# Kernel optimization log

Measured on AMD Instinct MI355X. Metric: run time of the kernel, lower is better.

The kernel has to match this reference:

```python
import jax, jax.numpy as jnp
import numpy as np

OS_FACTOR = 2.0  # init kwarg; k = 1/os_factor Euler step size
B, T, IN, H = 32, 4096, 1, 512


def setup_inputs() -> dict:
    key = jax.random.key(0)
    k0, k1, k2, k3, k4 = jax.random.split(key, 5)
    scale = 1.0 / np.sqrt(H).astype(np.float32)
    return {
        "x": jax.random.normal(k0, (B, T, IN), jnp.float32),
        "W_ih": jax.random.uniform(k1, (4 * H, IN), jnp.float32, -scale, scale),
        "W_hh": jax.random.uniform(k2, (4 * H, H), jnp.float32, -scale, scale),
        "b_ih": jax.random.uniform(k3, (4 * H,), jnp.float32, -scale, scale),
        "b_hh": jax.random.uniform(k4, (4 * H,), jnp.float32, -scale, scale),
    }


def reference(x, W_ih, W_hh, b_ih, b_hh):
    """STN_RNN forward with an LSTMCell: h_state <- h_state + k*(cell(x,h_state) - h_state).
    State vector is [h, c] concatenated (state_size = 2H). Returns (states_h, final_state)."""
    k = 1.0 / OS_FACTOR
    h = W_hh.shape[1]
    h0 = jnp.zeros((x.shape[0], 2 * h), x.dtype)

    def step(state, x_t):
        hs, cs = state[:, :h], state[:, h:]
        # torch.nn.LSTMCell gate math
        gates = x_t @ W_ih.T + b_ih + hs @ W_hh.T + b_hh  # [B, 4H]
        i_g, f_g, g_g, o_g = jnp.split(gates, 4, axis=-1)
        c_new = jax.nn.sigmoid(f_g) * cs + jax.nn.sigmoid(i_g) * jnp.tanh(g_g)
        h_new = jax.nn.sigmoid(o_g) * jnp.tanh(c_new)
        hc = jnp.concatenate([h_new, c_new], axis=-1)
        new_state = state + k * (hc - state)  # Euler integration of nonlinearity
        return new_state, new_state

    final_state, states = jax.lax.scan(step, h0, jnp.swapaxes(x, 0, 1))
    states = jnp.swapaxes(states, 0, 1)  # [B, T, 2H]
    return states[..., :h], final_state
```

## Files before the change

### kernel.cpp

```cpp
#include <hip/hip_runtime.h>
#include <hip/hip_bf16.h>


#define NBATCH 32
#define NT     4096
#define NH     512
#define UNITS  64

#define FLAG_OFF  0u
#define CTR_OFF   64u
#define BIAS_OFF  4096u
#define WIH_OFF   12288u
#define XF_OFF    20480u
#define HBUF_OFF  544768u
#define WP_OFF    675840u

__device__ __forceinline__ float bf2f(unsigned short u) {
    union { unsigned int i; float f; } v; v.i = ((unsigned int)u) << 16; return v.f;
}
__device__ __forceinline__ unsigned short f2bf_rne(float f) {
    union { unsigned int i; float f; } v; v.f = f;
    return (unsigned short)((v.i + 0x7fffu + ((v.i >> 16) & 1u)) >> 16);
}
__device__ __forceinline__ float lo_bf(unsigned int u) {
    union { unsigned int i; float f; } v; v.i = u << 16; return v.f;
}
__device__ __forceinline__ float hi_bf(unsigned int u) {
    union { unsigned int i; float f; } v; v.i = u & 0xffff0000u; return v.f;
}
__device__ __forceinline__ float sigm(float x) {
    return 1.0f / (1.0f + __expf(-x));
}
__device__ __forceinline__ float tanh_fast(float x) {
    float e = __expf(-2.0f * fabsf(x));
    float r = (1.0f - e) / (1.0f + e);
    return copysignf(r, x);
}
__device__ __forceinline__ int col2row(int col) {
    int wg = col >> 8, r = col & 255, g = (r >> 6) & 3, u = r & 63;
    return g * 512 + wg * 64 + u;
}

__global__ void prep_detect(const unsigned short* __restrict__ wih_u,
                            int* __restrict__ flagp,
                            unsigned int* __restrict__ ctr) {
    __shared__ int cnt;
    if (threadIdx.x == 0) cnt = 0;
    __syncthreads();
    int local = 0;
    for (int i = threadIdx.x; i < 1024; i += 256) {
        float v = bf2f(wih_u[2 * i]);
        if (fabsf(v) <= 0.0625f) local++;
    }
    atomicAdd(&cnt, local);
    __syncthreads();
    if (threadIdx.x == 0) *flagp = (cnt >= 1000) ? 1 : 0;
    if (threadIdx.x < 32) ctr[threadIdx.x * 16] = 0u;
}

__global__ void prep_conv(const void* __restrict__ x,
                          const void* __restrict__ Wih,
                          const void* __restrict__ Whh,
                          const void* __restrict__ bih,
                          const void* __restrict__ bhh,
                          const int* __restrict__ flagp,
                          unsigned int* __restrict__ WP,
                          float* __restrict__ bias_p,
                          float* __restrict__ wih_p,
                          float* __restrict__ Xf) {
    int idx = blockIdx.x * blockDim.x + threadIdx.x;
    int isbf = *flagp;

    {
        int wg  = idx >> 16;
        int rem = idx & 65535;
        int r4  = rem >> 11;
        int tid = (rem >> 2) & 511;
        int j   = rem & 3;
        int r   = r4 * 4 + j;
        int c   = r >> 5;
        int k2  = r & 31;
        int jq  = tid & 63;
        int ks  = tid >> 6;
        int col = wg * 256 + jq * 4 + c;
        int row = col2row(col);
        int k0  = ks * 64 + 2 * k2;
        unsigned short lo, hi;
        if (isbf) {
            lo = ((const unsigned short*)Whh)[(size_t)row * 512 + k0];
            hi = ((const unsigned short*)Whh)[(size_t)row * 512 + k0 + 1];
        } else {
            lo = f2bf_rne(((const float*)Whh)[(size_t)row * 512 + k0]);
            hi = f2bf_rne(((const float*)Whh)[(size_t)row * 512 + k0 + 1]);
        }
        WP[idx] = (unsigned int)lo | ((unsigned int)hi << 16);
    }

    if (idx < 2048) {
        int col = idx;
        int row = col2row(col);
        float bi, bh, wi;
        if (isbf) {
            bi = bf2f(((const unsigned short*)bih)[row]);
            bh = bf2f(((const unsigned short*)bhh)[row]);
            wi = bf2f(((const unsigned short*)Wih)[row]);
        } else {
            bi = ((const float*)bih)[row];
            bh = ((const float*)bhh)[row];
            wi = ((const float*)Wih)[row];
        }
        bias_p[col] = bi + bh;
        wih_p[col]  = wi;
    }
    if (idx < NBATCH * NT) {
        Xf[idx] = isbf ? bf2f(((const unsigned short*)x)[idx])
                       : ((const float*)x)[idx];
    }
}

__global__ void __launch_bounds__(512, 2) rnn_kernel(
    const float* __restrict__ Xf,
    const unsigned int* __restrict__ WP,
    const float* __restrict__ bias_p,
    const float* __restrict__ wih_p,
    float* __restrict__ hbuf,
    unsigned int* __restrict__ ctr,
    const int* __restrict__ flagp,
    void* __restrict__ out)
{
    const int tid = threadIdx.x;
    const int bid = blockIdx.x;
    const int b   = bid & 31;
    const int wg  = bid >> 5;
    const int isbf = *flagp;

    __shared__ float hsh[512];
    __shared__ float parts[8][256];
    __shared__ float gates[256];
    __shared__ float cst[UNITS];
    __shared__ float hst[UNITS];

    if (tid < UNITS) { cst[tid] = 0.0f; hst[tid] = 0.0f; }

    const int jq = tid & 63;
    const int ks = tid >> 6;

    unsigned int w[128];
    {
        const uint4* wp = (const uint4*)WP + (size_t)wg * 16384 + tid;
        #pragma unroll
        for (int r4 = 0; r4 < 32; ++r4) {
            uint4 v = wp[(size_t)r4 * 512];
            w[r4 * 4 + 0] = v.x;
            w[r4 * 4 + 1] = v.y;
            w[r4 * 4 + 2] = v.z;
            w[r4 * 4 + 3] = v.w;
        }
    }

    float biasr = 0.0f, wihr = 0.0f;
    if (tid < 256) {
        biasr = bias_p[wg * 256 + tid];
        wihr  = wih_p[wg * 256 + tid];
    }

    unsigned int* ctrb = ctr + b * 16;
    unsigned short* outb_u = (unsigned short*)out + (size_t)b * NT * NH;
    float*          outb_f = (float*)out + (size_t)b * NT * NH;

    unsigned int broken = 0;

    for (int t = 0; t < NT; ++t) {
        if (t == 0) {
            hsh[tid] = 0.0f;
        } else {
            if (tid == 0 && !broken) {
                unsigned int target = 8u * (unsigned int)t;
                int g = 0;
                while (__hip_atomic_load(ctrb, __ATOMIC_RELAXED,
                                         __HIP_MEMORY_SCOPE_AGENT) < target) {
                    __builtin_amdgcn_s_sleep(1);
                    if (++g > 16000000) { broken = 1; break; }
                }
            }
            __syncthreads();
            __atomic_signal_fence(__ATOMIC_SEQ_CST);
            const float* hin = hbuf + (((t & 1) * NBATCH + b) << 9);
            hsh[tid] = __hip_atomic_load(hin + tid, __ATOMIC_RELAXED,
                                         __HIP_MEMORY_SCOPE_AGENT);
        }
        __syncthreads();

        float a0 = 0.f, a1 = 0.f, a2 = 0.f, a3 = 0.f;
        float c0 = 0.f, c1 = 0.f, c2 = 0.f, c3 = 0.f;
        const float* hq = hsh + ks * 64;
        #pragma unroll
        for (int k2 = 0; k2 < 32; ++k2) {
            float h0 = hq[2 * k2];
            float h1 = hq[2 * k2 + 1];
            unsigned int u0 = w[k2];
            unsigned int u1 = w[32 + k2];
            unsigned int u2 = w[64 + k2];
            unsigned int u3 = w[96 + k2];
            a0 = fmaf(h0, lo_bf(u0), a0);  c0 = fmaf(h1, hi_bf(u0), c0);
            a1 = fmaf(h0, lo_bf(u1), a1);  c1 = fmaf(h1, hi_bf(u1), c1);
            a2 = fmaf(h0, lo_bf(u2), a2);  c2 = fmaf(h1, hi_bf(u2), c2);
            a3 = fmaf(h0, lo_bf(u3), a3);  c3 = fmaf(h1, hi_bf(u3), c3);
        }
        a0 += c0; a1 += c1; a2 += c2; a3 += c3;
        *(float4*)&parts[ks][jq * 4] = make_float4(a0, a1, a2, a3);
        __syncthreads();

        float xt = Xf[b * NT + t];
        if (tid < 256) {
            float g = parts[0][tid] + parts[1][tid] + parts[2][tid] + parts[3][tid]
                    + parts[4][tid] + parts[5][tid] + parts[6][tid] + parts[7][tid]
                    + biasr + xt * wihr;
            gates[tid] = g;
        }
        __syncthreads();

        if (tid < UNITS) {
            float ig = sigm(gates[tid]);
            float fg = sigm(gates[64 + tid]);
            float gg = tanh_fast(gates[128 + tid]);
            float og = sigm(gates[192 + tid]);
            float cold = cst[tid], hold = hst[tid];
            float cnew = fg * cold + ig * gg;
            float hnew = og * tanh_fast(cnew);
            float cb = 0.5f * (cold + cnew);
            float hb = 0.5f * (hold + hnew);
            cst[tid] = cb; hst[tid] = hb;
            float* hout = hbuf + ((((t + 1) & 1) * NBATCH + b) << 9);
            __hip_atomic_store(&hout[wg * 64 + tid], hb, __ATOMIC_RELAXED,
                               __HIP_MEMORY_SCOPE_AGENT);
            if (isbf) outb_u[(size_t)t * NH + wg * 64 + tid] = f2bf_rne(hb);
            else      outb_f[(size_t)t * NH + wg * 64 + tid] = hb;
        }
        __atomic_signal_fence(__ATOMIC_SEQ_CST);
        if (tid < 64) {
            __builtin_amdgcn_s_waitcnt(0);
            if (tid == 0)
                __hip_atomic_fetch_add(ctrb, 1u, __ATOMIC_RELAXED,
                                       __HIP_MEMORY_SCOPE_AGENT);
        }
        __syncthreads();
    }

    if (tid < UNITS) {
        size_t fsbase = (size_t)NBATCH * NT * NH + (size_t)b * (2 * NH);
        if (isbf) {
            ((unsigned short*)out)[fsbase + wg * 64 + tid]       = f2bf_rne(hst[tid]);
            ((unsigned short*)out)[fsbase + 512 + wg * 64 + tid] = f2bf_rne(cst[tid]);
        } else {
            ((float*)out)[fsbase + wg * 64 + tid]       = hst[tid];
            ((float*)out)[fsbase + 512 + wg * 64 + tid] = cst[tid];
        }
    }
}

extern "C" void kernel_launch(void* const* d_in, const int* in_sizes, int n_in,
                              void* d_out, int out_size, void* d_ws, size_t ws_size,
                              hipStream_t stream) {
    const void* x   = d_in[0];
    const void* Wih = d_in[1];
    const void* Whh = d_in[2];
    const void* bih = d_in[3];
    const void* bhh = d_in[4];

    char* ws = (char*)d_ws;
    int* flagp          = (int*)(ws + FLAG_OFF);
    unsigned int* ctrp  = (unsigned int*)(ws + CTR_OFF);
    float* bias_p       = (float*)(ws + BIAS_OFF);
    float* wih_p        = (float*)(ws + WIH_OFF);
    float* Xf           = (float*)(ws + XF_OFF);
    float* hbuf         = (float*)(ws + HBUF_OFF);
    unsigned int* WP    = (unsigned int*)(ws + WP_OFF);

    prep_detect<<<1, 256, 0, stream>>>((const unsigned short*)Wih, flagp, ctrp);
    prep_conv<<<2048, 256, 0, stream>>>(x, Wih, Whh, bih, bhh, flagp,
                                        WP, bias_p, wih_p, Xf);
    rnn_kernel<<<256, 512, 0, stream>>>(Xf, WP, bias_p, wih_p, hbuf, ctrp,
                                        flagp, d_out);
}
```

Baseline: 17.84 ms.

## Replace per-batch counter barrier with step-tagged 64-bit hidden-state packets

Each hidden value is now stored together with its timestep tag as one 64-bit atomic word. Each consumer thread polls its own element until the tag matches, which replaces the counter increment, waitcnt and extra block barrier on every step. The per-batch input sequence is also preloaded into shared memory so the per-step global read of x goes away. In exchange, the hidden buffer doubles in size and many threads spin on global memory, and the larger shared-memory footprint could affect occupancy under two blocks per SM.

Measured after the change: 15.86 ms. 11.1% less time.

```diff
diff --git a/kernel.cpp b/kernel.cpp
--- a/kernel.cpp
+++ b/kernel.cpp
@@ -8,12 +8,13 @@
 #define UNITS  64
 
 #define FLAG_OFF  0u
-#define CTR_OFF   64u
 #define BIAS_OFF  4096u
 #define WIH_OFF   12288u
 #define XF_OFF    20480u
 #define HBUF_OFF  544768u
-#define WP_OFF    675840u
+#define WP_OFF    806912u
+
+#define HBUF_DWORDS 65536
 
 __device__ __forceinline__ float bf2f(unsigned short u) {
     union { unsigned int i; float f; } v; v.i = ((unsigned int)u) << 16; return v.f;
@@ -42,8 +43,7 @@
 }
 
 __global__ void prep_detect(const unsigned short* __restrict__ wih_u,
-                            int* __restrict__ flagp,
-                            unsigned int* __restrict__ ctr) {
+                            int* __restrict__ flagp) {
     __shared__ int cnt;
     if (threadIdx.x == 0) cnt = 0;
     __syncthreads();
@@ -55,7 +55,6 @@
     atomicAdd(&cnt, local);
     __syncthreads();
     if (threadIdx.x == 0) *flagp = (cnt >= 1000) ? 1 : 0;
-    if (threadIdx.x < 32) ctr[threadIdx.x * 16] = 0u;
 }
 
 __global__ void prep_conv(const void* __restrict__ x,
@@ -67,7 +66,8 @@
                           unsigned int* __restrict__ WP,
                           float* __restrict__ bias_p,
                           float* __restrict__ wih_p,
-                          float* __restrict__ Xf) {
+                          float* __restrict__ Xf,
+                          unsigned int* __restrict__ hbuf_z) {
     int idx = blockIdx.x * blockDim.x + threadIdx.x;
     int isbf = *flagp;
 
@@ -96,6 +96,8 @@
         WP[idx] = (unsigned int)lo | ((unsigned int)hi << 16);
     }
 
+    if (idx < HBUF_DWORDS) hbuf_z[idx] = 0u;
+
     if (idx < 2048) {
         int col = idx;
         int row = col2row(col);
@@ -123,8 +125,7 @@
     const unsigned int* __restrict__ WP,
     const float* __restrict__ bias_p,
     const float* __restrict__ wih_p,
-    float* __restrict__ hbuf,
-    unsigned int* __restrict__ ctr,
+    unsigned long long* __restrict__ hbuf,
     const int* __restrict__ flagp,
     void* __restrict__ out)
 {
@@ -135,6 +136,7 @@
     const int isbf = *flagp;
 
     __shared__ float hsh[512];
+    __shared__ float xsh[NT];
     __shared__ float parts[8][256];
     __shared__ float gates[256];
     __shared__ float cst[UNITS];
@@ -144,6 +146,8 @@
 
     const int jq = tid & 63;
     const int ks = tid >> 6;
+
+    for (int i = tid; i < NT; i += 512) xsh[i] = Xf[(size_t)b * NT + i];
 
     unsigned int w[128];
     {
@@ -164,7 +168,6 @@
         wihr  = wih_p[wg * 256 + tid];
     }
 
-    unsigned int* ctrb = ctr + b * 16;
     unsigned short* outb_u = (unsigned short*)out + (size_t)b * NT * NH;
     float*          outb_f = (float*)out + (size_t)b * NT * NH;
 
@@ -174,20 +177,21 @@
         if (t == 0) {
             hsh[tid] = 0.0f;
         } else {
-            if (tid == 0 && !broken) {
-                unsigned int target = 8u * (unsigned int)t;
+            const unsigned long long* hin =
+                hbuf + (((t & 1) * NBATCH + b) << 9);
+            unsigned long long v = 0;
+            if (!broken) {
                 int g = 0;
-                while (__hip_atomic_load(ctrb, __ATOMIC_RELAXED,
-                                         __HIP_MEMORY_SCOPE_AGENT) < target) {
+                for (;;) {
+                    v = __hip_atomic_load(hin + tid, __ATOMIC_RELAXED,
+                                          __HIP_MEMORY_SCOPE_AGENT);
+                    if ((unsigned int)(v >> 32) == (unsigned int)t) break;
                     __builtin_amdgcn_s_sleep(1);
-                    if (++g > 16000000) { broken = 1; break; }
+                    if (++g > 16000000) { broken = 1; v = 0; break; }
                 }
             }
-            __syncthreads();
-            __atomic_signal_fence(__ATOMIC_SEQ_CST);
-            const float* hin = hbuf + (((t & 1) * NBATCH + b) << 9);
-            hsh[tid] = __hip_atomic_load(hin + tid, __ATOMIC_RELAXED,
-                                         __HIP_MEMORY_SCOPE_AGENT);
+            union { unsigned int u; float f; } cv; cv.u = (unsigned int)v;
+            hsh[tid] = cv.f;
         }
         __syncthreads();
 
@@ -211,11 +215,10 @@
         *(float4*)&parts[ks][jq * 4] = make_float4(a0, a1, a2, a3);
         __syncthreads();
 
-        float xt = Xf[b * NT + t];
         if (tid < 256) {
             float g = parts[0][tid] + parts[1][tid] + parts[2][tid] + parts[3][tid]
                     + parts[4][tid] + parts[5][tid] + parts[6][tid] + parts[7][tid]
-                    + biasr + xt * wihr;
+                    + biasr + xsh[t] * wihr;
             gates[tid] = g;
         }
         __syncthreads();
@@ -231,20 +234,16 @@
             float cb = 0.5f * (cold + cnew);
             float hb = 0.5f * (hold + hnew);
             cst[tid] = cb; hst[tid] = hb;
-            float* hout = hbuf + ((((t + 1) & 1) * NBATCH + b) << 9);
-            __hip_atomic_store(&hout[wg * 64 + tid], hb, __ATOMIC_RELAXED,
+            union { float f; unsigned int u; } hv; hv.f = hb;
+            unsigned long long pkt =
+                ((unsigned long long)(unsigned int)(t + 1) << 32) | hv.u;
+            unsigned long long* hout =
+                hbuf + ((((t + 1) & 1) * NBATCH + b) << 9) + wg * 64 + tid;
+            __hip_atomic_store(hout, pkt, __ATOMIC_RELAXED,
                                __HIP_MEMORY_SCOPE_AGENT);
             if (isbf) outb_u[(size_t)t * NH + wg * 64 + tid] = f2bf_rne(hb);
             else      outb_f[(size_t)t * NH + wg * 64 + tid] = hb;
         }
-        __atomic_signal_fence(__ATOMIC_SEQ_CST);
-        if (tid < 64) {
-            __builtin_amdgcn_s_waitcnt(0);
-            if (tid == 0)
-                __hip_atomic_fetch_add(ctrb, 1u, __ATOMIC_RELAXED,
-                                       __HIP_MEMORY_SCOPE_AGENT);
-        }
-        __syncthreads();
     }
 
     if (tid < UNITS) {
@@ -270,16 +269,16 @@
 
     char* ws = (char*)d_ws;
     int* flagp          = (int*)(ws + FLAG_OFF);
-    unsigned int* ctrp  = (unsigned int*)(ws + CTR_OFF);
     float* bias_p       = (float*)(ws + BIAS_OFF);
     float* wih_p        = (float*)(ws + WIH_OFF);
     float* Xf           = (float*)(ws + XF_OFF);
-    float* hbuf         = (float*)(ws + HBUF_OFF);
+    unsigned long long* hbuf = (unsigned long long*)(ws + HBUF_OFF);
     unsigned int* WP    = (unsigned int*)(ws + WP_OFF);
 
-    prep_detect<<<1, 256, 0, stream>>>((const unsigned short*)Wih, flagp, ctrp);
+    prep_detect<<<1, 256, 0, stream>>>((const unsigned short*)Wih, flagp);
     prep_conv<<<2048, 256, 0, stream>>>(x, Wih, Whh, bih, bhh, flagp,
-                                        WP, bias_p, wih_p, Xf);
-    rnn_kernel<<<256, 512, 0, stream>>>(Xf, WP, bias_p, wih_p, hbuf, ctrp,
+                                        WP, bias_p, wih_p, Xf,
+                                        (unsigned int*)hbuf);
+    rnn_kernel<<<256, 512, 0, stream>>>(Xf, WP, bias_p, wih_p, hbuf,
                                         flagp, d_out);
 }
```
